# Optimization experiments

Hardware: AMD Instinct MI355X
Metric: run time of the kernel (lower is better)

Reference implementation:

```python
import jax, jax.numpy as jnp
import numpy as np

HIDDEN = 4096
NUM_HEADS = 32
HEAD_DIM = HIDDEN // NUM_HEADS  # 128
ROPE_THETA = 10000.0
MAX_POS = 2048


def _rope_tables():
    inv_freq = 1.0 / (ROPE_THETA ** (jnp.arange(0, HEAD_DIM, 2, dtype=jnp.float32) / HEAD_DIM))
    t = jnp.arange(MAX_POS, dtype=jnp.float32)
    freqs = jnp.einsum('i,j->ij', t, inv_freq)          # [MAX_POS, HEAD_DIM/2]
    emb = jnp.concatenate([freqs, freqs], axis=-1)      # [MAX_POS, HEAD_DIM]
    return jnp.cos(emb), jnp.sin(emb)


def _apply_rotary(x, cos, sin):
    # x: [b, s, h, d]; cos/sin: [b, s, 1, d]
    half = x.shape[-1] // 2
    x_rot = jnp.concatenate([-x[..., half:], x[..., :half]], axis=-1)
    return x * cos + x_rot * sin


def setup_inputs() -> dict:
    key = jax.random.key(0)
    k1, k2, k3, k4, k5 = jax.random.split(key, 5)
    B, S = 1, 2048
    scale = 1.0 / np.sqrt(HIDDEN)
    return {
        'hidden_states': jax.random.normal(k1, (B, S, HIDDEN), dtype=jnp.float32),
        'position_ids': jnp.arange(S, dtype=jnp.int64).reshape(1, S),
        'wqkv_w': jax.random.normal(k2, (3 * HIDDEN, HIDDEN), dtype=jnp.float32) * scale,
        'wqkv_b': jax.random.normal(k3, (3 * HIDDEN,), dtype=jnp.float32) * 0.01,
        'wo_w': jax.random.normal(k4, (HIDDEN, HIDDEN), dtype=jnp.float32) * scale,
        'wo_b': jax.random.normal(k5, (HIDDEN,), dtype=jnp.float32) * 0.01,
    }


def reference(hidden_states, position_ids, wqkv_w, wqkv_b, wo_w, wo_b):
    b, s, _ = hidden_states.shape
    qkv = hidden_states @ wqkv_w.T + wqkv_b                  # [b, s, 3*hidden]
    qkv = qkv.reshape(b, s, NUM_HEADS, 3, HEAD_DIM)          # (h g d) layout
    q, k, v = qkv[..., 0, :], qkv[..., 1, :], qkv[..., 2, :]  # [b, s, h, d]

    cos_tab, sin_tab = _rope_tables()
    cos = cos_tab[position_ids][:, :, None, :]               # [b_or_1, s, 1, d]
    sin = sin_tab[position_ids][:, :, None, :]
    q = _apply_rotary(q, cos, sin)
    k = _apply_rotary(k, cos, sin)

    scores = jnp.einsum('bqhd,bkhd->bhqk', q, k) / jnp.sqrt(jnp.float32(HEAD_DIM))
    causal = jnp.tril(jnp.ones((s, s), dtype=bool))
    scores = jnp.where(causal[None, None, :, :], scores, -jnp.inf)
    attn = jax.nn.softmax(scores, axis=-1)
    out = jnp.einsum('bhqk,bkhd->bqhd', attn, v).reshape(b, s, HIDDEN)
    return out @ wo_w.T + wo_b
```

## Files before the change

### kernel.cpp

```cpp
#include <hip/hip_runtime.h>
#include <hip/hip_bf16.h>

typedef short bf16x8 __attribute__((ext_vector_type(8)));
typedef float f32x4  __attribute__((ext_vector_type(4)));

typedef __attribute__((address_space(1))) const unsigned int gu32_t;
typedef __attribute__((address_space(3))) unsigned int lu32_t;

__device__ inline void gld16(const void* g, void* l) {
  __builtin_amdgcn_global_load_lds((gu32_t*)g, (lu32_t*)l, 16, 0, 0);
}

__device__ inline float bf2f(__hip_bfloat16 x) { return __bfloat162float(x); }

#define S_LEN 2048
#define HID   4096
#define NH    32
#define HD    128
#define QKV_N 12288

__global__ void cvt_bf16_kernel(const float* __restrict__ in,
                                __hip_bfloat16* __restrict__ out, long n) {
  long stride = (long)gridDim.x * blockDim.x;
  for (long i = (long)blockIdx.x * blockDim.x + threadIdx.x; i * 8 < n; i += stride) {
    long b = i * 8;
    float4 a0 = *(const float4*)(in + b);
    float4 a1 = *(const float4*)(in + b + 4);
    union { __hip_bfloat16 h[8]; bf16x8 v; } u;
    u.h[0] = __float2bfloat16(a0.x); u.h[1] = __float2bfloat16(a0.y);
    u.h[2] = __float2bfloat16(a0.z); u.h[3] = __float2bfloat16(a0.w);
    u.h[4] = __float2bfloat16(a1.x); u.h[5] = __float2bfloat16(a1.y);
    u.h[6] = __float2bfloat16(a1.z); u.h[7] = __float2bfloat16(a1.w);
    *(bf16x8*)(out + b) = u.v;
  }
}

template<int WRITE_BF16>
__global__ __launch_bounds__(256) void gemm_bt_kernel(
    const __hip_bfloat16* __restrict__ A,
    const __hip_bfloat16* __restrict__ B,
    const float* __restrict__ bias,
    void* __restrict__ Cout, int M, int N, int K)
{
  __shared__ __hip_bfloat16 lA[128 * 64];
  __shared__ __hip_bfloat16 lB[128 * 64];
  const int t = threadIdx.x;
  const int w = t >> 6, l = t & 63;
  const int lr = l & 15, lg = l >> 4;
  const int nwg = gridDim.x * gridDim.y;
  const int bid = blockIdx.y * gridDim.x + blockIdx.x;
  const int swz = (bid & 7) * (nwg >> 3) + (bid >> 3);
  const int m0 = (swz % gridDim.x) * 128, n0 = (swz / gridDim.x) * 128;
  const int wm = (w >> 1) * 64, wn = (w & 1) * 64;

  f32x4 acc[4][4] = {};

  for (int k0 = 0; k0 < K; k0 += 64) {
    #pragma unroll
    for (int i = 0; i < 4; ++i) {
      int c = i * 256 + t;
      int row = c >> 3, s = c & 7;
      gld16(A + (long)(m0 + row) * K + k0 + (s ^ (row & 7)) * 8, &lA[c * 8]);
    }
    #pragma unroll
    for (int i = 0; i < 4; ++i) {
      int c = i * 256 + t;
      int row = c >> 3, s = c & 7;
      gld16(B + (long)(n0 + row) * K + k0 + (s ^ (row & 7)) * 8, &lB[c * 8]);
    }
    __syncthreads();
    #pragma unroll
    for (int ks = 0; ks < 2; ++ks) {
      bf16x8 af[4], bfr[4];
      #pragma unroll
      for (int mi = 0; mi < 4; ++mi) {
        int row = wm + mi * 16 + lr;
        af[mi] = *(const bf16x8*)&lA[row * 64 + ((ks * 4 + lg) ^ (row & 7)) * 8];
      }
      #pragma unroll
      for (int ni = 0; ni < 4; ++ni) {
        int row = wn + ni * 16 + lr;
        bfr[ni] = *(const bf16x8*)&lB[row * 64 + ((ks * 4 + lg) ^ (row & 7)) * 8];
      }
      #pragma unroll
      for (int mi = 0; mi < 4; ++mi)
        #pragma unroll
        for (int ni = 0; ni < 4; ++ni)
          acc[mi][ni] = __builtin_amdgcn_mfma_f32_16x16x32_bf16(af[mi], bfr[ni], acc[mi][ni], 0, 0, 0);
    }
    __syncthreads();
  }

  #pragma unroll
  for (int mi = 0; mi < 4; ++mi) {
    #pragma unroll
    for (int ni = 0; ni < 4; ++ni) {
      int col = n0 + wn + ni * 16 + lr;
      float bv = bias[col];
      #pragma unroll
      for (int r = 0; r < 4; ++r) {
        int row = m0 + wm + mi * 16 + lg * 4 + r;
        float v = acc[mi][ni][r] + bv;
        if (WRITE_BF16)
          ((__hip_bfloat16*)Cout)[(long)row * N + col] = __float2bfloat16(v);
        else
          ((float*)Cout)[(long)row * N + col] = v;
      }
    }
  }
}

__global__ void rope_table_kernel(const int* __restrict__ pos,
                                  float* __restrict__ ct, float* __restrict__ st) {
  int s = blockIdx.x, j = threadIdx.x;
  float p = (float)pos[s];
  float invf = exp2f(-0.20762050593046013f * (float)j);
  float a = p * invf;
  ct[s * 64 + j] = cosf(a);
  st[s * 64 + j] = sinf(a);
}

__global__ __launch_bounds__(256) void rope_rearrange_kernel(
    const __hip_bfloat16* __restrict__ qkv,
    const float* __restrict__ ct, const float* __restrict__ st,
    __hip_bfloat16* __restrict__ Qr, __hip_bfloat16* __restrict__ Kr,
    __hip_bfloat16* __restrict__ Vt)
{
  __shared__ __hip_bfloat16 lv[64][136];
  const int h = blockIdx.y, s0 = blockIdx.x * 64, t = threadIdx.x;

  #pragma unroll
  for (int half = 0; half < 2; ++half) {
    int si = half * 32 + (t >> 3);
    int jo = (t & 7) * 8;
    long base = (long)(s0 + si) * QKV_N + h * 384;
    union { __hip_bfloat16 h8[8]; bf16x8 v; } q1, q2, k1, k2, o;
    q1.v = *(const bf16x8*)(qkv + base + jo);
    q2.v = *(const bf16x8*)(qkv + base + 64 + jo);
    k1.v = *(const bf16x8*)(qkv + base + 128 + jo);
    k2.v = *(const bf16x8*)(qkv + base + 192 + jo);
    const float* cp = ct + (s0 + si) * 64 + jo;
    const float* sp = st + (s0 + si) * 64 + jo;
    long ob = (long)h * (S_LEN * HD) + (long)(s0 + si) * HD;
    #pragma unroll
    for (int e = 0; e < 8; ++e)
      o.h8[e] = __float2bfloat16(bf2f(q1.h8[e]) * cp[e] - bf2f(q2.h8[e]) * sp[e]);
    *(bf16x8*)(Qr + ob + jo) = o.v;
    #pragma unroll
    for (int e = 0; e < 8; ++e)
      o.h8[e] = __float2bfloat16(bf2f(q2.h8[e]) * cp[e] + bf2f(q1.h8[e]) * sp[e]);
    *(bf16x8*)(Qr + ob + 64 + jo) = o.v;
    #pragma unroll
    for (int e = 0; e < 8; ++e)
      o.h8[e] = __float2bfloat16(bf2f(k1.h8[e]) * cp[e] - bf2f(k2.h8[e]) * sp[e]);
    *(bf16x8*)(Kr + ob + jo) = o.v;
    #pragma unroll
    for (int e = 0; e < 8; ++e)
      o.h8[e] = __float2bfloat16(bf2f(k2.h8[e]) * cp[e] + bf2f(k1.h8[e]) * sp[e]);
    *(bf16x8*)(Kr + ob + 64 + jo) = o.v;
    *(bf16x8*)&lv[si][jo]      = *(const bf16x8*)(qkv + base + 256 + jo);
    *(bf16x8*)&lv[si][64 + jo] = *(const bf16x8*)(qkv + base + 320 + jo);
  }
  __syncthreads();
  #pragma unroll
  for (int i = 0; i < 4; ++i) {
    int c = i * 256 + t;
    int d = c >> 3, s8 = (c & 7) * 8;
    union { __hip_bfloat16 h8[8]; bf16x8 v; } u;
    #pragma unroll
    for (int j2 = 0; j2 < 8; ++j2) u.h8[j2] = lv[s8 + j2][d];
    *(bf16x8*)(Vt + (long)h * (HD * S_LEN) + (long)d * S_LEN + s0 + s8) = u.v;
  }
}

#define FA_STAGE(buf, k0_) do {                                              \
    _Pragma("unroll")                                                        \
    for (int i_ = 0; i_ < 4; ++i_) {               \
      int c_ = i_ * 256 + t;                                                 \
      int row_ = c_ >> 4, s_ = c_ & 15;                                      \
      gld16(Kh + (long)((k0_) + row_) * HD + (s_ ^ (row_ & 15)) * 8,         \
            &lK[buf][c_ * 8]);                                               \
    }                                                                        \
    _Pragma("unroll")                                                        \
    for (int i_ = 0; i_ < 4; ++i_) {             \
      int c_ = i_ * 256 + t;                                                 \
      int d_ = c_ >> 3, s_ = c_ & 7;                                         \
      gld16(Vh + (long)d_ * S_LEN + (k0_) + (s_ ^ (d_ & 7)) * 8,             \
            &lV[buf][c_ * 8]);                                               \
    } } while (0)

__global__ __launch_bounds__(256) void flash_attn_kernel(
    const __hip_bfloat16* __restrict__ Qr, const __hip_bfloat16* __restrict__ Kr,
    const __hip_bfloat16* __restrict__ Vt, __hip_bfloat16* __restrict__ O)
{
  __shared__ __hip_bfloat16 lK[2][64 * 128];
  __shared__ __hip_bfloat16 lV[2][128 * 64];
  __shared__ __hip_bfloat16 lP[4][16 * 72];
  const int h = blockIdx.y, pair = blockIdx.x;
  const int t = threadIdx.x, w = t >> 6, l = t & 63;
  const int lr = l & 15, lg = l >> 4;
  const __hip_bfloat16* Qh = Qr + (long)h * (S_LEN * HD);
  const __hip_bfloat16* Kh = Kr + (long)h * (S_LEN * HD);
  const __hip_bfloat16* Vh = Vt + (long)h * (HD * S_LEN);
  const float sc2 = 0.12751744f;

  for (int ph = 0; ph < 2; ++ph) {
    const int qt = ph ? (31 - pair) : pair;
    const int q0 = qt * 64;

    bf16x8 qf[4];
    #pragma unroll
    for (int ks = 0; ks < 4; ++ks)
      qf[ks] = *(const bf16x8*)(Qh + (long)(q0 + w * 16 + lr) * HD + ks * 32 + lg * 8);

    float m_r[4], l_r[4];
    f32x4 oacc[8] = {};
    #pragma unroll
    for (int r = 0; r < 4; ++r) { m_r[r] = -1e30f; l_r[r] = 0.f; }

    const int ktiles = qt + 1;
    int cur = 0;
    FA_STAGE(0, 0);
    __syncthreads();

    for (int kt = 0; kt < ktiles; ++kt) {
      const int k0 = kt * 64;
      if (kt + 1 < ktiles) FA_STAGE(cur ^ 1, k0 + 64);

      f32x4 s[4] = {};
      #pragma unroll
      for (int ks = 0; ks < 4; ++ks) {
        bf16x8 kf[4];
        #pragma unroll
        for (int nf = 0; nf < 4; ++nf) {
          int row = nf * 16 + lr;
          kf[nf] = *(const bf16x8*)&lK[cur][row * 128 + ((ks * 4 + lg) ^ (row & 15)) * 8];
        }
        #pragma unroll
        for (int nf = 0; nf < 4; ++nf)
          s[nf] = __builtin_amdgcn_mfma_f32_16x16x32_bf16(qf[ks], kf[nf], s[nf], 0, 0, 0);
      }

      if (kt == qt) {
        #pragma unroll
        for (int nf = 0; nf < 4; ++nf) {
          int k = k0 + nf * 16 + lr;
          #pragma unroll
          for (int r = 0; r < 4; ++r) {
            int q = q0 + w * 16 + lg * 4 + r;
            float v = s[nf][r] * sc2;
            s[nf][r] = (k > q) ? -1e30f : v;
          }
        }
      } else {
        #pragma unroll
        for (int nf = 0; nf < 4; ++nf)
          #pragma unroll
          for (int r = 0; r < 4; ++r)
            s[nf][r] *= sc2;
      }

      bool need = false;
      float lm[4];
      #pragma unroll
      for (int r = 0; r < 4; ++r) {
        lm[r] = fmaxf(fmaxf(s[0][r], s[1][r]), fmaxf(s[2][r], s[3][r]));
        need = need || (lm[r] > m_r[r] + 8.f);
      }
      if (__any((int)need)) {
        #pragma unroll
        for (int r = 0; r < 4; ++r) {
          float mx = lm[r];
          #pragma unroll
          for (int mk = 1; mk < 16; mk <<= 1) mx = fmaxf(mx, __shfl_xor(mx, mk));
          float mo = m_r[r];
          float mn = fmaxf(mo, mx);
          float alpha = exp2f(mo - mn);
          m_r[r] = mn;
          l_r[r] *= alpha;
          #pragma unroll
          for (int df = 0; df < 8; ++df) oacc[df][r] *= alpha;
        }
      }

      #pragma unroll
      for (int r = 0; r < 4; ++r) {
        float rs = 0.f;
        #pragma unroll
        for (int nf = 0; nf < 4; ++nf) {
          float p = exp2f(s[nf][r] - m_r[r]);
          s[nf][r] = p;
          rs += p;
        }
        #pragma unroll
        for (int mk = 1; mk < 16; mk <<= 1) rs += __shfl_xor(rs, mk);
        l_r[r] += rs;
      }

      #pragma unroll
      for (int nf = 0; nf < 4; ++nf)
        #pragma unroll
        for (int r = 0; r < 4; ++r)
          lP[w][(lg * 4 + r) * 72 + nf * 16 + lr] = __float2bfloat16(s[nf][r]);
      asm volatile("s_waitcnt lgkmcnt(0)" ::: "memory");

      #pragma unroll
      for (int ks2 = 0; ks2 < 2; ++ks2) {
        bf16x8 pa = *(const bf16x8*)&lP[w][lr * 72 + ks2 * 32 + lg * 8];
        #pragma unroll
        for (int df = 0; df < 8; ++df) {
          int row = df * 16 + lr;
          bf16x8 vf = *(const bf16x8*)&lV[cur][row * 64 + ((ks2 * 4 + lg) ^ (row & 7)) * 8];
          oacc[df] = __builtin_amdgcn_mfma_f32_16x16x32_bf16(pa, vf, oacc[df], 0, 0, 0);
        }
      }
      __syncthreads();
      cur ^= 1;
    }

    #pragma unroll
    for (int r = 0; r < 4; ++r) {
      float inv = 1.f / l_r[r];
      long q = q0 + w * 16 + lg * 4 + r;
      #pragma unroll
      for (int df = 0; df < 8; ++df)
        O[q * HID + h * HD + df * 16 + lr] = __float2bfloat16(oacc[df][r] * inv);
    }
    __syncthreads();
  }
}

extern "C" void kernel_launch(void* const* d_in, const int* in_sizes, int n_in,
                              void* d_out, int out_size, void* d_ws, size_t ws_size,
                              hipStream_t stream)
{
  (void)in_sizes; (void)n_in; (void)out_size;
  const float* hidden = (const float*)d_in[0];
  const int*   pos    = (const int*)d_in[1];
  const float* wqkv_w = (const float*)d_in[2];
  const float* wqkv_b = (const float*)d_in[3];
  const float* wo_w   = (const float*)d_in[4];
  const float* wo_b   = (const float*)d_in[5];
  float* out = (float*)d_out;

  char* ws = (char*)d_ws;
  if (ws_size < 167772160UL) return;
  __hip_bfloat16* hid_bf  = (__hip_bfloat16*)(ws + 0);
  __hip_bfloat16* wqkv_bf = (__hip_bfloat16*)(ws + 16777216);
  __hip_bfloat16* qr      = (__hip_bfloat16*)(ws + 0);
  __hip_bfloat16* kr      = (__hip_bfloat16*)(ws + 16777216);
  __hip_bfloat16* vt      = (__hip_bfloat16*)(ws + 33554432);
  __hip_bfloat16* obf     = (__hip_bfloat16*)(ws + 50331648);
  __hip_bfloat16* wo_bf   = (__hip_bfloat16*)(ws + 67108864);
  float*          cos_t   = (float*)(ws + 100663296);
  float*          sin_t   = (float*)(ws + 100663296 + 524288);
  __hip_bfloat16* qkv_bf  = (__hip_bfloat16*)(ws + 117440512);

  cvt_bf16_kernel<<<4096, 256, 0, stream>>>(hidden, hid_bf, 8388608L);
  cvt_bf16_kernel<<<8192, 256, 0, stream>>>(wqkv_w, wqkv_bf, 50331648L);
  gemm_bt_kernel<1><<<dim3(16, 96), 256, 0, stream>>>(hid_bf, wqkv_bf, wqkv_b, qkv_bf, 2048, 12288, 4096);
  cvt_bf16_kernel<<<8192, 256, 0, stream>>>(wo_w, wo_bf, 16777216L);
  rope_table_kernel<<<2048, 64, 0, stream>>>(pos, cos_t, sin_t);
  rope_rearrange_kernel<<<dim3(32, 32), 256, 0, stream>>>(qkv_bf, cos_t, sin_t, qr, kr, vt);
  flash_attn_kernel<<<dim3(16, 32), 256, 0, stream>>>(qr, kr, vt, obf);
  gemm_bt_kernel<0><<<dim3(16, 32), 256, 0, stream>>>(obf, wo_bf, wo_b, out, 2048, 4096, 4096);
}
```

Before: 478.9 us.

## Double query tile per flash-attention block to reuse K/V tiles across two row groups

Each wave now handles 32 query rows (two 16-row MFMA fragments) instead of 16, so a block covers 128 queries and each K/V tile loaded into LDS feeds twice as many MFMAs. The grid shrinks from 16x32 to 8x32 blocks, with causal pairing adjusted to 16 query tiles. This halves K/V global/LDS traffic per query, at the cost of more registers (doubled accumulators and softmax state) and fewer blocks (256 on a 256-CU GPU), which may reduce occupancy and load balance.

```diff
diff --git a/kernel.cpp b/kernel.cpp
--- a/kernel.cpp
+++ b/kernel.cpp
@@ -195,7 +195,7 @@
 {
   __shared__ __hip_bfloat16 lK[2][64 * 128];
   __shared__ __hip_bfloat16 lV[2][128 * 64];
-  __shared__ __hip_bfloat16 lP[4][16 * 72];
+  __shared__ __hip_bfloat16 lP[4][32 * 72];
   const int h = blockIdx.y, pair = blockIdx.x;
   const int t = threadIdx.x, w = t >> 6, l = t & 63;
   const int lr = l & 15, lg = l >> 4;
@@ -205,20 +205,24 @@
   const float sc2 = 0.12751744f;
 
   for (int ph = 0; ph < 2; ++ph) {
-    const int qt = ph ? (31 - pair) : pair;
-    const int q0 = qt * 64;
-
-    bf16x8 qf[4];
-    #pragma unroll
-    for (int ks = 0; ks < 4; ++ks)
-      qf[ks] = *(const bf16x8*)(Qh + (long)(q0 + w * 16 + lr) * HD + ks * 32 + lg * 8);
-
-    float m_r[4], l_r[4];
-    f32x4 oacc[8] = {};
-    #pragma unroll
-    for (int r = 0; r < 4; ++r) { m_r[r] = -1e30f; l_r[r] = 0.f; }
-
-    const int ktiles = qt + 1;
+    const int qt = ph ? (15 - pair) : pair;
+    const int q0 = qt * 128;
+
+    bf16x8 qf[2][4];
+    #pragma unroll
+    for (int mi = 0; mi < 2; ++mi)
+      #pragma unroll
+      for (int ks = 0; ks < 4; ++ks)
+        qf[mi][ks] = *(const bf16x8*)(Qh + (long)(q0 + w * 32 + mi * 16 + lr) * HD + ks * 32 + lg * 8);
+
+    float m_r[2][4], l_r[2][4];
+    f32x4 oacc[2][8] = {};
+    #pragma unroll
+    for (int mi = 0; mi < 2; ++mi)
+      #pragma unroll
+      for (int r = 0; r < 4; ++r) { m_r[mi][r] = -1e30f; l_r[mi][r] = 0.f; }
+
+    const int ktiles = 2 * qt + 2;
     int cur = 0;
     FA_STAGE(0, 0);
     __syncthreads();
@@ -227,7 +231,7 @@
       const int k0 = kt * 64;
       if (kt + 1 < ktiles) FA_STAGE(cur ^ 1, k0 + 64);
 
-      f32x4 s[4] = {};
+      f32x4 s[2][4] = {};
       #pragma unroll
       for (int ks = 0; ks < 4; ++ks) {
         bf16x8 kf[4];
@@ -237,81 +241,97 @@
           kf[nf] = *(const bf16x8*)&lK[cur][row * 128 + ((ks * 4 + lg) ^ (row & 15)) * 8];
         }
         #pragma unroll
+        for (int mi = 0; mi < 2; ++mi)
+          #pragma unroll
+          for (int nf = 0; nf < 4; ++nf)
+            s[mi][nf] = __builtin_amdgcn_mfma_f32_16x16x32_bf16(qf[mi][ks], kf[nf], s[mi][nf], 0, 0, 0);
+      }
+
+      if (kt >= 2 * qt) {
+        #pragma unroll
+        for (int mi = 0; mi < 2; ++mi)
+          #pragma unroll
+          for (int nf = 0; nf < 4; ++nf) {
+            int k = k0 + nf * 16 + lr;
+            #pragma unroll
+            for (int r = 0; r < 4; ++r) {
+              int q = q0 + w * 32 + mi * 16 + lg * 4 + r;
+              float v = s[mi][nf][r] * sc2;
+              s[mi][nf][r] = (k > q) ? -1e30f : v;
+            }
+          }
+      } else {
+        #pragma unroll
+        for (int mi = 0; mi < 2; ++mi)
+          #pragma unroll
+          for (int nf = 0; nf < 4; ++nf)
+            #pragma unroll
+            for (int r = 0; r < 4; ++r)
+              s[mi][nf][r] *= sc2;
+      }
+
+      bool need = false;
+      float lm[2][4];
+      #pragma unroll
+      for (int mi = 0; mi < 2; ++mi)
+        #pragma unroll
+        for (int r = 0; r < 4; ++r) {
+          lm[mi][r] = fmaxf(fmaxf(s[mi][0][r], s[mi][1][r]), fmaxf(s[mi][2][r], s[mi][3][r]));
+          need = need || (lm[mi][r] > m_r[mi][r] + 8.f);
+        }
+      if (__any((int)need)) {
+        #pragma unroll
+        for (int mi = 0; mi < 2; ++mi)
+          #pragma unroll
+          for (int r = 0; r < 4; ++r) {
+            float mx = lm[mi][r];
+            #pragma unroll
+            for (int mk = 1; mk < 16; mk <<= 1) mx = fmaxf(mx, __shfl_xor(mx, mk));
+            float mo = m_r[mi][r];
+            float mn = fmaxf(mo, mx);
+            float alpha = exp2f(mo - mn);
+            m_r[mi][r] = mn;
+            l_r[mi][r] *= alpha;
+            #pragma unroll
+            for (int df = 0; df < 8; ++df) oacc[mi][df][r] *= alpha;
+          }
+      }
+
+      #pragma unroll
+      for (int mi = 0; mi < 2; ++mi)
+        #pragma unroll
+        for (int r = 0; r < 4; ++r) {
+          float rs = 0.f;
+          #pragma unroll
+          for (int nf = 0; nf < 4; ++nf) {
+            float p = exp2f(s[mi][nf][r] - m_r[mi][r]);
+            s[mi][nf][r] = p;
+            rs += p;
+          }
+          #pragma unroll
+          for (int mk = 1; mk < 16; mk <<= 1) rs += __shfl_xor(rs, mk);
+          l_r[mi][r] += rs;
+        }
+
+      #pragma unroll
+      for (int mi = 0; mi < 2; ++mi)
+        #pragma unroll
         for (int nf = 0; nf < 4; ++nf)
-          s[nf] = __builtin_amdgcn_mfma_f32_16x16x32_bf16(qf[ks], kf[nf], s[nf], 0, 0, 0);
-      }
-
-      if (kt == qt) {
-        #pragma unroll
-        for (int nf = 0; nf < 4; ++nf) {
-          int k = k0 + nf * 16 + lr;
-          #pragma unroll
-          for (int r = 0; r < 4; ++r) {
-            int q = q0 + w * 16 + lg * 4 + r;
-            float v = s[nf][r] * sc2;
-            s[nf][r] = (k > q) ? -1e30f : v;
-          }
-        }
-      } else {
-        #pragma unroll
-        for (int nf = 0; nf < 4; ++nf)
           #pragma unroll
           for (int r = 0; r < 4; ++r)
-            s[nf][r] *= sc2;
-      }
-
-      bool need = false;
-      float lm[4];
-      #pragma unroll
-      for (int r = 0; r < 4; ++r) {
-        lm[r] = fmaxf(fmaxf(s[0][r], s[1][r]), fmaxf(s[2][r], s[3][r]));
-        need = need || (lm[r] > m_r[r] + 8.f);
-      }
-      if (__any((int)need)) {
-        #pragma unroll
-        for (int r = 0; r < 4; ++r) {
-          float mx = lm[r];
-          #pragma unroll
-          for (int mk = 1; mk < 16; mk <<= 1) mx = fmaxf(mx, __shfl_xor(mx, mk));
-          float mo = m_r[r];
-          float mn = fmaxf(mo, mx);
-          float alpha = exp2f(mo - mn);
-          m_r[r] = mn;
-          l_r[r] *= alpha;
-          #pragma unroll
-          for (int df = 0; df < 8; ++df) oacc[df][r] *= alpha;
-        }
-      }
-
-      #pragma unroll
-      for (int r = 0; r < 4; ++r) {
-        float rs = 0.f;
-        #pragma unroll
-        for (int nf = 0; nf < 4; ++nf) {
-          float p = exp2f(s[nf][r] - m_r[r]);
-          s[nf][r] = p;
-          rs += p;
-        }
-        #pragma unroll
-        for (int mk = 1; mk < 16; mk <<= 1) rs += __shfl_xor(rs, mk);
-        l_r[r] += rs;
-      }
-
-      #pragma unroll
-      for (int nf = 0; nf < 4; ++nf)
-        #pragma unroll
-        for (int r = 0; r < 4; ++r)
-          lP[w][(lg * 4 + r) * 72 + nf * 16 + lr] = __float2bfloat16(s[nf][r]);
+            lP[w][(mi * 16 + lg * 4 + r) * 72 + nf * 16 + lr] = __float2bfloat16(s[mi][nf][r]);
       asm volatile("s_waitcnt lgkmcnt(0)" ::: "memory");
 
       #pragma unroll
       for (int ks2 = 0; ks2 < 2; ++ks2) {
-        bf16x8 pa = *(const bf16x8*)&lP[w][lr * 72 + ks2 * 32 + lg * 8];
+        bf16x8 pa0 = *(const bf16x8*)&lP[w][lr * 72 + ks2 * 32 + lg * 8];
+        bf16x8 pa1 = *(const bf16x8*)&lP[w][(16 + lr) * 72 + ks2 * 32 + lg * 8];
         #pragma unroll
         for (int df = 0; df < 8; ++df) {
           int row = df * 16 + lr;
           bf16x8 vf = *(const bf16x8*)&lV[cur][row * 64 + ((ks2 * 4 + lg) ^ (row & 7)) * 8];
-          oacc[df] = __builtin_amdgcn_mfma_f32_16x16x32_bf16(pa, vf, oacc[df], 0, 0, 0);
+          oacc[0][df] = __builtin_amdgcn_mfma_f32_16x16x32_bf16(pa0, vf, oacc[0][df], 0, 0, 0);
+          oacc[1][df] = __builtin_amdgcn_mfma_f32_16x16x32_bf16(pa1, vf, oacc[1][df], 0, 0, 0);
         }
       }
       __syncthreads();
@@ -319,13 +339,15 @@
     }
 
     #pragma unroll
-    for (int r = 0; r < 4; ++r) {
-      float inv = 1.f / l_r[r];
-      long q = q0 + w * 16 + lg * 4 + r;
-      #pragma unroll
-      for (int df = 0; df < 8; ++df)
-        O[q * HID + h * HD + df * 16 + lr] = __float2bfloat16(oacc[df][r] * inv);
-    }
+    for (int mi = 0; mi < 2; ++mi)
+      #pragma unroll
+      for (int r = 0; r < 4; ++r) {
+        float inv = 1.f / l_r[mi][r];
+        long q = q0 + w * 32 + mi * 16 + lg * 4 + r;
+        #pragma unroll
+        for (int df = 0; df < 8; ++df)
+          O[q * HID + h * HD + df * 16 + lr] = __float2bfloat16(oacc[mi][df][r] * inv);
+      }
     __syncthreads();
   }
 }
@@ -362,6 +384,6 @@
   cvt_bf16_kernel<<<8192, 256, 0, stream>>>(wo_w, wo_bf, 16777216L);
   rope_table_kernel<<<2048, 64, 0, stream>>>(pos, cos_t, sin_t);
   rope_rearrange_kernel<<<dim3(32, 32), 256, 0, stream>>>(qkv_bf, cos_t, sin_t, qr, kr, vt);
-  flash_attn_kernel<<<dim3(16, 32), 256, 0, stream>>>(qr, kr, vt, obf);
+  flash_attn_kernel<<<dim3(8, 32), 256, 0, stream>>>(qr, kr, vt, obf);
   gemm_bt_kernel<0><<<dim3(16, 32), 256, 0, stream>>>(obf, wo_bf, wo_b, out, 2048, 4096, 4096);
 }
```

Result: slower. 496.9 us (+3.7%).
